# Kernel optimization log

Hardware: AMD Instinct MI355X
Metric: run time of the kernel (lower is better)

## Reference

```python
import jax, jax.numpy as jnp
import numpy as np

V, D, H, DFF, L = 32000, 256, 4, 1024, 4
B, T = 2, 2048
DK = D // H
EPS = 1e-5


def setup_inputs() -> dict:
    key = jax.random.key(0)
    ks = jax.random.split(key, 8)
    s = 0.02
    return {
        "tokens": jax.random.randint(ks[0], (B, T), 0, V),
        "embed": jax.random.normal(ks[1], (V, D), jnp.float32) * s,
        "qkv_w": jax.random.normal(ks[2], (L, 3 * D, D), jnp.float32) * s,
        "qkv_b": jnp.zeros((L, 3 * D), jnp.float32),
        "fc_w": jax.random.normal(ks[3], (L, D, D), jnp.float32) * s,
        "fc_b": jnp.zeros((L, D), jnp.float32),
        "ln1_s": jnp.ones((L, D), jnp.float32),
        "ln1_b": jnp.zeros((L, D), jnp.float32),
        "w1": jax.random.normal(ks[4], (L, DFF, D), jnp.float32) * s,
        "b1": jnp.zeros((L, DFF), jnp.float32),
        "w2": jax.random.normal(ks[5], (L, D, DFF), jnp.float32) * s,
        "b2": jnp.zeros((L, D), jnp.float32),
        "ln2_s": jnp.ones((L, D), jnp.float32),
        "ln2_b": jnp.zeros((L, D), jnp.float32),
        "lnf_s": jnp.ones((D,), jnp.float32),
        "lnf_b": jnp.zeros((D,), jnp.float32),
        "out_w": jax.random.normal(ks[6], (V, D), jnp.float32) * s,
        "out_b": jnp.zeros((V,), jnp.float32),
    }


def _layernorm(x, s, b):
    mu = jnp.mean(x, axis=-1, keepdims=True)
    var = jnp.mean(jnp.square(x - mu), axis=-1, keepdims=True)
    return (x - mu) * jax.lax.rsqrt(var + EPS) * s + b


def _pos_encoding(t, d):
    pos = jnp.arange(t, dtype=jnp.float32)[:, None]
    div = jnp.exp(jnp.arange(0, d, 2, dtype=jnp.float32) * (-np.log(10000.0) / d))
    pe = jnp.zeros((t, d), jnp.float32)
    pe = pe.at[:, 0::2].set(jnp.sin(pos * div))
    pe = pe.at[:, 1::2].set(jnp.cos(pos * div))
    return pe


def reference(tokens, embed, qkv_w, qkv_b, fc_w, fc_b, ln1_s, ln1_b,
              w1, b1, w2, b2, ln2_s, ln2_b, lnf_s, lnf_b, out_w, out_b):
    b, t = tokens.shape
    x = embed[tokens] + _pos_encoding(t, D)[None]  # [B,T,D]
    causal = jnp.tril(jnp.ones((t, t), bool))
    scale = 1.0 / np.sqrt(DK)
    for l in range(L):
        # --- attention ---
        qkv = jnp.einsum('btd,ed->bte', x, qkv_w[l]) + qkv_b[l]  # [B,T,3D]
        qkv = qkv.reshape(b, t, 3, H, DK)
        q, k, v = qkv[:, :, 0], qkv[:, :, 1], qkv[:, :, 2]  # [B,T,H,DK]
        scores = jnp.einsum('bqhd,bkhd->bhqk', q, k) * scale
        scores = jnp.where(causal, scores, -jnp.inf)
        attn = jax.nn.softmax(scores, axis=-1)
        o = jnp.einsum('bhqk,bkhd->bqhd', attn, v).reshape(b, t, D)
        o = jnp.einsum('btd,ed->bte', o, fc_w[l]) + fc_b[l]
        x = _layernorm(x + o, ln1_s[l], ln1_b[l])
        # --- feed-forward ---
        h = jax.nn.relu(jnp.einsum('btd,fd->btf', x, w1[l]) + b1[l])
        f = jnp.einsum('btf,df->btd', h, w2[l]) + b2[l]
        x = _layernorm(x + f, ln2_s[l], ln2_b[l])
    x = _layernorm(x, lnf_s, lnf_b)
    logits = jnp.einsum('btd,vd->btv', x, out_w) + out_b
    return logits
```

## Files before the change

### kernel.cpp

```cpp
#include <hip/hip_runtime.h>
#include <math.h>

typedef __attribute__((ext_vector_type(8))) short bf16x8;
typedef __attribute__((ext_vector_type(4))) float f32x4;
typedef __attribute__((ext_vector_type(4))) unsigned int u32x4;
typedef __attribute__((ext_vector_type(4))) unsigned short u16x4;

static constexpr int Tn = 2048;
static constexpr int Dm = 256;
static constexpr int NHn = 4;
static constexpr int Ln = 4;
static constexpr int DFFn = 1024;
static constexpr int Vn = 32000;
static constexpr int BTn = 4096;

__device__ __forceinline__ unsigned short f2bf(float f) {
  unsigned int u = __float_as_uint(f);
  u += 0x7fffu + ((u >> 16) & 1u);
  return (unsigned short)(u >> 16);
}

__device__ __forceinline__ void gld_lds16(const unsigned short* g, unsigned short* l) {
  __builtin_amdgcn_global_load_lds((const __attribute__((address_space(1))) unsigned int*)g,
                                   (__attribute__((address_space(3))) unsigned int*)l, 16, 0, 0);
}

__global__ __launch_bounds__(256) void cvt_f2bf(const float* __restrict__ in,
                                                unsigned short* __restrict__ out, int n) {
  int i = (blockIdx.x * 256 + threadIdx.x) * 4;
  if (i >= n) return;
  float4 v = *reinterpret_cast<const float4*>(in + i);
  u16x4 o;
  o[0] = f2bf(v.x); o[1] = f2bf(v.y); o[2] = f2bf(v.z); o[3] = f2bf(v.w);
  *reinterpret_cast<u16x4*>(out + i) = o;
}

__global__ __launch_bounds__(256) void embed_pos(const int* __restrict__ tokens,
                                                 const float* __restrict__ emb,
                                                 float* __restrict__ xf,
                                                 unsigned short* __restrict__ xb) {
  int idx = blockIdx.x * 256 + threadIdx.x;
  int bt = idx >> 8, d = idx & 255;
  int t = bt & (Tn - 1);
  int tok = tokens[bt];
  float v = emb[(size_t)tok * Dm + d];
  int i2 = d & ~1;
  float dv = expf((float)i2 * (-0.03597789207803249f));
  float arg = (float)t * dv;
  float pe = (d & 1) ? cosf(arg) : sinf(arg);
  float x = v + pe;
  xf[idx] = x;
  xb[idx] = f2bf(x);
}

__global__ __launch_bounds__(256) void add_ln(const float* __restrict__ addend,
                                              const float* __restrict__ gam,
                                              const float* __restrict__ bet,
                                              float* __restrict__ xf,
                                              unsigned short* __restrict__ xb) {
  int row = blockIdx.x, d = threadIdx.x;
  __shared__ float red[8];
  size_t off = (size_t)row * Dm + d;
  float u = xf[off];
  if (addend) u += addend[off];
  float tsum = u;
  #pragma unroll
  for (int o = 32; o > 0; o >>= 1) tsum += __shfl_xor(tsum, o);
  int w = d >> 6, lane = d & 63;
  if (lane == 0) red[w] = tsum;
  __syncthreads();
  float mean = (red[0] + red[1] + red[2] + red[3]) * (1.f / 256.f);
  float df = u - mean;
  float vsum = df * df;
  #pragma unroll
  for (int o = 32; o > 0; o >>= 1) vsum += __shfl_xor(vsum, o);
  if (lane == 0) red[4 + w] = vsum;
  __syncthreads();
  float var = (red[4] + red[5] + red[6] + red[7]) * (1.f / 256.f);
  float y = df * rsqrtf(var + 1e-5f) * gam[d] + bet[d];
  xf[off] = y;
  xb[off] = f2bf(y);
}

__global__ __launch_bounds__(256) void attn_mfma(const unsigned short* __restrict__ qkv,
                                                 unsigned short* __restrict__ ob) {
  int lin = blockIdx.y * gridDim.x + blockIdx.x;
  int wg = (lin & 7) * 32 + (lin >> 3);
  int qb = wg & 31, bh = wg >> 5;
  int b = bh >> 2, h = bh & 3;
  int q0 = qb * 64;
  int tid = threadIdx.x;
  int lane = tid & 63, w = tid >> 6;
  int l15 = lane & 15, quad = lane >> 4;

  __shared__ __align__(16) unsigned short Ps[4][16 * 64];
  __shared__ __align__(16) unsigned short Vt[64 * 64];

  const size_t rowQ = (size_t)(b * Tn + q0 + w * 16 + l15) * 768 + h * 64 + quad * 8;
  bf16x8 aq0 = *reinterpret_cast<const bf16x8*>(qkv + rowQ);
  bf16x8 aq1 = *reinterpret_cast<const bf16x8*>(qkv + rowQ + 32);

  float m_i[4], l_i[4];
  f32x4 oacc[4];
  #pragma unroll
  for (int i = 0; i < 4; i++) { m_i[i] = -INFINITY; l_i[i] = 0.f; oacc[i] = (f32x4){0.f, 0.f, 0.f, 0.f}; }

  for (int jt = 0; jt <= qb; jt++) {
    int j0 = jt * 64;
    __syncthreads();
    {
      int kv = tid & 63, g = tid >> 6;
      const unsigned short* vsrc = qkv + (size_t)(b * Tn + j0 + kv) * 768 + 512 + h * 64 + g * 16;
      bf16x8 v0 = *reinterpret_cast<const bf16x8*>(vsrc);
      bf16x8 v1 = *reinterpret_cast<const bf16x8*>(vsrc + 8);
      char* vb = (char*)Vt;
      #pragma unroll
      for (int j = 0; j < 8; j++) {
        int dk = g * 16 + j;
        *(unsigned short*)(vb + (((dk * 128 + kv * 2)) ^ ((dk & 7) << 4))) = (unsigned short)v0[j];
      }
      #pragma unroll
      for (int j = 0; j < 8; j++) {
        int dk = g * 16 + 8 + j;
        *(unsigned short*)(vb + (((dk * 128 + kv * 2)) ^ ((dk & 7) << 4))) = (unsigned short)v1[j];
      }
    }
    __syncthreads();

    f32x4 sc[4];
    const size_t rowK = (size_t)(b * Tn + j0 + l15) * 768 + 256 + h * 64 + quad * 8;
    #pragma unroll
    for (int f = 0; f < 4; f++) {
      bf16x8 bk0 = *reinterpret_cast<const bf16x8*>(qkv + rowK + (size_t)f * 16 * 768);
      bf16x8 bk1 = *reinterpret_cast<const bf16x8*>(qkv + rowK + (size_t)f * 16 * 768 + 32);
      f32x4 a = (f32x4){0.f, 0.f, 0.f, 0.f};
      a = __builtin_amdgcn_mfma_f32_16x16x32_bf16(aq0, bk0, a, 0, 0, 0);
      a = __builtin_amdgcn_mfma_f32_16x16x32_bf16(aq1, bk1, a, 0, 0, 0);
      sc[f] = a;
    }

    bool diag = (jt == qb);
    float alpha[4];
    #pragma unroll
    for (int rr = 0; rr < 4; rr++) {
      int qg = q0 + w * 16 + quad * 4 + rr;
      float sv[4];
      #pragma unroll
      for (int f = 0; f < 4; f++) {
        sv[f] = sc[f][rr] * 0.125f;
        if (diag && (j0 + f * 16 + l15 > qg)) sv[f] = -INFINITY;
      }
      float mx = fmaxf(fmaxf(sv[0], sv[1]), fmaxf(sv[2], sv[3]));
      #pragma unroll
      for (int o = 8; o > 0; o >>= 1) mx = fmaxf(mx, __shfl_xor(mx, o));
      float mnew = fmaxf(m_i[rr], mx);
      float p[4], ps = 0.f;
      #pragma unroll
      for (int f = 0; f < 4; f++) { p[f] = __expf(sv[f] - mnew); ps += p[f]; }
      #pragma unroll
      for (int o = 8; o > 0; o >>= 1) ps += __shfl_xor(ps, o);
      alpha[rr] = __expf(m_i[rr] - mnew);
      l_i[rr] = l_i[rr] * alpha[rr] + ps;
      m_i[rr] = mnew;
      int qq = quad * 4 + rr;
      char* pb = (char*)Ps[w];
      #pragma unroll
      for (int f = 0; f < 4; f++)
        *(unsigned short*)(pb + (((qq * 128 + (f * 16 + l15) * 2)) ^ ((qq & 7) << 4))) = f2bf(p[f]);
    }

    #pragma unroll
    for (int ni = 0; ni < 4; ni++)
      #pragma unroll
      for (int rr = 0; rr < 4; rr++) oacc[ni][rr] *= alpha[rr];

    bf16x8 pa[2];
    {
      char* pb = (char*)Ps[w];
      #pragma unroll
      for (int kc = 0; kc < 2; kc++)
        pa[kc] = *reinterpret_cast<const bf16x8*>(
            pb + (((l15 * 128 + kc * 64 + quad * 16)) ^ ((l15 & 7) << 4)));
    }
    char* vb = (char*)Vt;
    #pragma unroll
    for (int ni = 0; ni < 4; ni++) {
      int dk = ni * 16 + l15;
      #pragma unroll
      for (int kc = 0; kc < 2; kc++) {
        bf16x8 bv = *reinterpret_cast<const bf16x8*>(
            vb + (((dk * 128 + kc * 64 + quad * 16)) ^ ((dk & 7) << 4)));
        oacc[ni] = __builtin_amdgcn_mfma_f32_16x16x32_bf16(pa[kc], bv, oacc[ni], 0, 0, 0);
      }
    }
  }

  #pragma unroll
  for (int ni = 0; ni < 4; ni++) {
    #pragma unroll
    for (int rr = 0; rr < 4; rr++) {
      int qg = q0 + w * 16 + quad * 4 + rr;
      float o = oacc[ni][rr] / l_i[rr];
      ob[(size_t)(b * Tn + qg) * Dm + h * 64 + ni * 16 + l15] = f2bf(o);
    }
  }
}

template <int BM, int EPI>
__global__ __launch_bounds__(256) void gemm_bt(const unsigned short* __restrict__ A,
                                               const unsigned short* __restrict__ W,
                                               const float* __restrict__ bias,
                                               float* __restrict__ Cf,
                                               unsigned short* __restrict__ Cb,
                                               int M, int N, int K) {
  constexpr int MI = BM / 32;
  __shared__ __align__(16) unsigned short As[BM * 32];
  __shared__ __align__(16) unsigned short Bs[128 * 32];
  int tid = threadIdx.x;
  int lane = tid & 63, w = tid >> 6;
  int wm = (w >> 1) * (BM / 2), wn = (w & 1) * 64;
  int r = lane & 15, quad = lane >> 4;

  int nwg = gridDim.x * gridDim.y;
  int lin = blockIdx.y * gridDim.x + blockIdx.x;
  int xcd = lin & 7, pos = lin >> 3;
  int qch = nwg >> 3, rch = nwg & 7;
  int wg = (xcd < rch ? xcd * (qch + 1) : rch * (qch + 1) + (xcd - rch) * qch) + pos;
  int m0 = (wg % gridDim.x) * BM;
  int n0 = (wg / gridDim.x) * 128;

  f32x4 acc[MI][4];
  #pragma unroll
  for (int i = 0; i < MI; i++)
    #pragma unroll
    for (int j = 0; j < 4; j++) acc[i][j] = (f32x4){0.f, 0.f, 0.f, 0.f};

  int lrow = lane >> 2;
  int lcol = (lane & 3) * 8;
  for (int k0 = 0; k0 < K; k0 += 32) {
    __syncthreads();
    #pragma unroll
    for (int i = 0; i < BM / 64; i++) {
      int rowA = i * 64 + w * 16;
      gld_lds16(A + (size_t)(m0 + rowA + lrow) * K + k0 + lcol, &As[rowA * 32]);
    }
    #pragma unroll
    for (int i = 0; i < 2; i++) {
      int rowB = i * 64 + w * 16;
      gld_lds16(W + (size_t)(n0 + rowB + lrow) * K + k0 + lcol, &Bs[rowB * 32]);
    }
    __syncthreads();
    bf16x8 af[MI], bfr[4];
    #pragma unroll
    for (int mi = 0; mi < MI; mi++)
      af[mi] = *reinterpret_cast<const bf16x8*>(&As[(wm + mi * 16 + r) * 32 + quad * 8]);
    #pragma unroll
    for (int ni = 0; ni < 4; ni++)
      bfr[ni] = *reinterpret_cast<const bf16x8*>(&Bs[(wn + ni * 16 + r) * 32 + quad * 8]);
    #pragma unroll
    for (int mi = 0; mi < MI; mi++)
      #pragma unroll
      for (int ni = 0; ni < 4; ni++)
        acc[mi][ni] = __builtin_amdgcn_mfma_f32_16x16x32_bf16(af[mi], bfr[ni], acc[mi][ni], 0, 0, 0);
  }
  #pragma unroll
  for (int mi = 0; mi < MI; mi++) {
    #pragma unroll
    for (int ni = 0; ni < 4; ni++) {
      int n = n0 + wn + ni * 16 + r;
      float bv = bias[n];
      #pragma unroll
      for (int rr = 0; rr < 4; rr++) {
        int m = m0 + wm + mi * 16 + quad * 4 + rr;
        float v = acc[mi][ni][rr] + bv;
        if (EPI == 0) {
          Cf[(size_t)m * N + n] = v;
        } else if (EPI == 1) {
          Cb[(size_t)m * N + n] = f2bf(fmaxf(v, 0.f));
        } else {
          Cb[(size_t)m * N + n] = f2bf(v);
        }
      }
    }
  }
}

extern "C" void kernel_launch(void* const* d_in, const int* in_sizes, int n_in,
                              void* d_out, int out_size, void* d_ws, size_t ws_size,
                              hipStream_t stream) {
  (void)in_sizes; (void)n_in; (void)out_size; (void)ws_size;
  const int* tokens = (const int*)d_in[0];
  const float* emb = (const float*)d_in[1];
  const float* qkv_w = (const float*)d_in[2];
  const float* qkv_b = (const float*)d_in[3];
  const float* fc_w = (const float*)d_in[4];
  const float* fc_b = (const float*)d_in[5];
  const float* ln1_s = (const float*)d_in[6];
  const float* ln1_b = (const float*)d_in[7];
  const float* w1 = (const float*)d_in[8];
  const float* b1 = (const float*)d_in[9];
  const float* w2 = (const float*)d_in[10];
  const float* b2 = (const float*)d_in[11];
  const float* ln2_s = (const float*)d_in[12];
  const float* ln2_b = (const float*)d_in[13];
  const float* lnf_s = (const float*)d_in[14];
  const float* lnf_b = (const float*)d_in[15];
  const float* out_w = (const float*)d_in[16];
  const float* out_b = (const float*)d_in[17];
  float* logits = (float*)d_out;

  char* p = (char*)d_ws;
  auto carve = [&](size_t bytes) {
    char* r = p;
    p += (bytes + 255) & ~(size_t)255;
    return r;
  };
  float* xf = (float*)carve((size_t)BTn * Dm * 4);
  unsigned short* xb = (unsigned short*)carve((size_t)BTn * Dm * 2);
  unsigned short* qkvb = (unsigned short*)carve((size_t)BTn * 768 * 2);
  unsigned short* obb = (unsigned short*)carve((size_t)BTn * Dm * 2);
  float* of = (float*)carve((size_t)BTn * Dm * 4);
  unsigned short* hb = (unsigned short*)carve((size_t)BTn * DFFn * 2);
  float* ff = (float*)carve((size_t)BTn * Dm * 4);
  unsigned short* wqkvb = (unsigned short*)carve((size_t)Ln * 768 * Dm * 2);
  unsigned short* wfcb = (unsigned short*)carve((size_t)Ln * Dm * Dm * 2);
  unsigned short* w1b = (unsigned short*)carve((size_t)Ln * DFFn * Dm * 2);
  unsigned short* w2b = (unsigned short*)carve((size_t)Ln * Dm * DFFn * 2);
  unsigned short* outwb = (unsigned short*)carve((size_t)Vn * Dm * 2);

  auto cvt = [&](const float* src, unsigned short* dst, int n) {
    cvt_f2bf<<<dim3((n / 4 + 255) / 256), dim3(256), 0, stream>>>(src, dst, n);
  };
  cvt(qkv_w, wqkvb, Ln * 768 * Dm);
  cvt(fc_w, wfcb, Ln * Dm * Dm);
  cvt(w1, w1b, Ln * DFFn * Dm);
  cvt(w2, w2b, Ln * Dm * DFFn);
  cvt(out_w, outwb, Vn * Dm);

  embed_pos<<<dim3(BTn), dim3(256), 0, stream>>>(tokens, emb, xf, xb);

  for (int l = 0; l < Ln; l++) {
    gemm_bt<64, 2><<<dim3(BTn / 64, 768 / 128), dim3(256), 0, stream>>>(
        xb, wqkvb + (size_t)l * 768 * Dm, qkv_b + l * 768, nullptr, qkvb, BTn, 768, Dm);
    attn_mfma<<<dim3(Tn / 64, 2 * NHn), dim3(256), 0, stream>>>(qkvb, obb);
    gemm_bt<64, 0><<<dim3(BTn / 64, Dm / 128), dim3(256), 0, stream>>>(
        obb, wfcb + (size_t)l * Dm * Dm, fc_b + l * Dm, of, nullptr, BTn, Dm, Dm);
    add_ln<<<dim3(BTn), dim3(256), 0, stream>>>(of, ln1_s + l * Dm, ln1_b + l * Dm, xf, xb);
    gemm_bt<128, 1><<<dim3(BTn / 128, DFFn / 128), dim3(256), 0, stream>>>(
        xb, w1b + (size_t)l * DFFn * Dm, b1 + l * DFFn, nullptr, hb, BTn, DFFn, Dm);
    gemm_bt<64, 0><<<dim3(BTn / 64, Dm / 128), dim3(256), 0, stream>>>(
        hb, w2b + (size_t)l * Dm * DFFn, b2 + l * Dm, ff, nullptr, BTn, Dm, DFFn);
    add_ln<<<dim3(BTn), dim3(256), 0, stream>>>(ff, ln2_s + l * Dm, ln2_b + l * Dm, xf, xb);
  }
  add_ln<<<dim3(BTn), dim3(256), 0, stream>>>(nullptr, lnf_s, lnf_b, xf, xb);

  gemm_bt<128, 0><<<dim3(BTn / 128, Vn / 128), dim3(256), 0, stream>>>(
      xb, outwb, out_b, logits, nullptr, BTn, Vn, Dm);
}
```

Before: 1.253 ms.

## Load GEMM operands directly to registers and fuse weight conversions into one launch

Replaces the LDS-staged GEMM with one where each wave loads its MFMA fragments straight from global memory into registers. K becomes a compile-time parameter with an unrolled k-loop, and all __syncthreads barriers are removed. The five weight-conversion launches are merged into one kernel, and the fc/w2 GEMMs use smaller M tiles to get more blocks. The aim is to cut barrier and launch overhead. The risk is redundant global and L2 traffic, because waves sharing rows no longer share loaded tiles, and the 16-byte fragment loads are strided.

```diff
diff --git a/kernel.cpp b/kernel.cpp
--- a/kernel.cpp
+++ b/kernel.cpp
@@ -20,19 +20,25 @@
   return (unsigned short)(u >> 16);
 }
 
-__device__ __forceinline__ void gld_lds16(const unsigned short* g, unsigned short* l) {
-  __builtin_amdgcn_global_load_lds((const __attribute__((address_space(1))) unsigned int*)g,
-                                   (__attribute__((address_space(3))) unsigned int*)l, 16, 0, 0);
-}
-
-__global__ __launch_bounds__(256) void cvt_f2bf(const float* __restrict__ in,
-                                                unsigned short* __restrict__ out, int n) {
-  int i = (blockIdx.x * 256 + threadIdx.x) * 4;
-  if (i >= n) return;
-  float4 v = *reinterpret_cast<const float4*>(in + i);
+__global__ __launch_bounds__(256) void cvt_all(const float* __restrict__ s0, unsigned short* __restrict__ d0,
+                                               const float* __restrict__ s1, unsigned short* __restrict__ d1,
+                                               const float* __restrict__ s2, unsigned short* __restrict__ d2,
+                                               const float* __restrict__ s3, unsigned short* __restrict__ d3,
+                                               const float* __restrict__ s4, unsigned short* __restrict__ d4,
+                                               int e0, int e1, int e2, int e3, int e4) {
+  int g = blockIdx.x * 256 + threadIdx.x;
+  if (g >= e4) return;
+  const float* s; unsigned short* d; int base;
+  if (g < e0)      { s = s0; d = d0; base = 0; }
+  else if (g < e1) { s = s1; d = d1; base = e0; }
+  else if (g < e2) { s = s2; d = d2; base = e1; }
+  else if (g < e3) { s = s3; d = d3; base = e2; }
+  else             { s = s4; d = d4; base = e3; }
+  int i = (g - base) * 4;
+  float4 v = *reinterpret_cast<const float4*>(s + i);
   u16x4 o;
   o[0] = f2bf(v.x); o[1] = f2bf(v.y); o[2] = f2bf(v.z); o[3] = f2bf(v.w);
-  *reinterpret_cast<u16x4*>(out + i) = o;
+  *reinterpret_cast<u16x4*>(d + i) = o;
 }
 
 __global__ __launch_bounds__(256) void embed_pos(const int* __restrict__ tokens,
@@ -206,28 +212,30 @@
   }
 }
 
-template <int BM, int EPI>
-__global__ __launch_bounds__(256) void gemm_bt(const unsigned short* __restrict__ A,
+template <int BM, int K, int EPI>
+__global__ __launch_bounds__(256) void gemm_rf(const unsigned short* __restrict__ A,
                                                const unsigned short* __restrict__ W,
                                                const float* __restrict__ bias,
                                                float* __restrict__ Cf,
                                                unsigned short* __restrict__ Cb,
-                                               int M, int N, int K) {
+                                               int N) {
   constexpr int MI = BM / 32;
-  __shared__ __align__(16) unsigned short As[BM * 32];
-  __shared__ __align__(16) unsigned short Bs[128 * 32];
   int tid = threadIdx.x;
   int lane = tid & 63, w = tid >> 6;
   int wm = (w >> 1) * (BM / 2), wn = (w & 1) * 64;
   int r = lane & 15, quad = lane >> 4;
 
-  int nwg = gridDim.x * gridDim.y;
-  int lin = blockIdx.y * gridDim.x + blockIdx.x;
+  int gx = gridDim.x;
+  int nwg = gx * gridDim.y;
+  int lin = blockIdx.y * gx + blockIdx.x;
   int xcd = lin & 7, pos = lin >> 3;
   int qch = nwg >> 3, rch = nwg & 7;
   int wg = (xcd < rch ? xcd * (qch + 1) : rch * (qch + 1) + (xcd - rch) * qch) + pos;
-  int m0 = (wg % gridDim.x) * BM;
-  int n0 = (wg / gridDim.x) * 128;
+  int m0 = (wg % gx) * BM;
+  int n0 = (wg / gx) * 128;
+
+  const unsigned short* Ap = A + (size_t)(m0 + wm + r) * K + quad * 8;
+  const unsigned short* Wp = W + (size_t)(n0 + wn + r) * K + quad * 8;
 
   f32x4 acc[MI][4];
   #pragma unroll
@@ -235,34 +243,22 @@
     #pragma unroll
     for (int j = 0; j < 4; j++) acc[i][j] = (f32x4){0.f, 0.f, 0.f, 0.f};
 
-  int lrow = lane >> 2;
-  int lcol = (lane & 3) * 8;
+  #pragma unroll 8
   for (int k0 = 0; k0 < K; k0 += 32) {
-    __syncthreads();
-    #pragma unroll
-    for (int i = 0; i < BM / 64; i++) {
-      int rowA = i * 64 + w * 16;
-      gld_lds16(A + (size_t)(m0 + rowA + lrow) * K + k0 + lcol, &As[rowA * 32]);
-    }
-    #pragma unroll
-    for (int i = 0; i < 2; i++) {
-      int rowB = i * 64 + w * 16;
-      gld_lds16(W + (size_t)(n0 + rowB + lrow) * K + k0 + lcol, &Bs[rowB * 32]);
-    }
-    __syncthreads();
     bf16x8 af[MI], bfr[4];
     #pragma unroll
     for (int mi = 0; mi < MI; mi++)
-      af[mi] = *reinterpret_cast<const bf16x8*>(&As[(wm + mi * 16 + r) * 32 + quad * 8]);
+      af[mi] = *reinterpret_cast<const bf16x8*>(Ap + (size_t)mi * 16 * K + k0);
     #pragma unroll
     for (int ni = 0; ni < 4; ni++)
-      bfr[ni] = *reinterpret_cast<const bf16x8*>(&Bs[(wn + ni * 16 + r) * 32 + quad * 8]);
+      bfr[ni] = *reinterpret_cast<const bf16x8*>(Wp + (size_t)ni * 16 * K + k0);
     #pragma unroll
     for (int mi = 0; mi < MI; mi++)
       #pragma unroll
       for (int ni = 0; ni < 4; ni++)
         acc[mi][ni] = __builtin_amdgcn_mfma_f32_16x16x32_bf16(af[mi], bfr[ni], acc[mi][ni], 0, 0, 0);
   }
+
   #pragma unroll
   for (int mi = 0; mi < MI; mi++) {
     #pragma unroll
@@ -328,32 +324,33 @@
   unsigned short* w2b = (unsigned short*)carve((size_t)Ln * Dm * DFFn * 2);
   unsigned short* outwb = (unsigned short*)carve((size_t)Vn * Dm * 2);
 
-  auto cvt = [&](const float* src, unsigned short* dst, int n) {
-    cvt_f2bf<<<dim3((n / 4 + 255) / 256), dim3(256), 0, stream>>>(src, dst, n);
-  };
-  cvt(qkv_w, wqkvb, Ln * 768 * Dm);
-  cvt(fc_w, wfcb, Ln * Dm * Dm);
-  cvt(w1, w1b, Ln * DFFn * Dm);
-  cvt(w2, w2b, Ln * Dm * DFFn);
-  cvt(out_w, outwb, Vn * Dm);
+  {
+    int c0 = Ln * 768 * Dm / 4;
+    int c1 = c0 + Ln * Dm * Dm / 4;
+    int c2 = c1 + Ln * DFFn * Dm / 4;
+    int c3 = c2 + Ln * Dm * DFFn / 4;
+    int c4 = c3 + Vn * Dm / 4;
+    cvt_all<<<dim3((c4 + 255) / 256), dim3(256), 0, stream>>>(
+        qkv_w, wqkvb, fc_w, wfcb, w1, w1b, w2, w2b, out_w, outwb, c0, c1, c2, c3, c4);
+  }
 
   embed_pos<<<dim3(BTn), dim3(256), 0, stream>>>(tokens, emb, xf, xb);
 
   for (int l = 0; l < Ln; l++) {
-    gemm_bt<64, 2><<<dim3(BTn / 64, 768 / 128), dim3(256), 0, stream>>>(
-        xb, wqkvb + (size_t)l * 768 * Dm, qkv_b + l * 768, nullptr, qkvb, BTn, 768, Dm);
+    gemm_rf<64, 256, 2><<<dim3(BTn / 64, 768 / 128), dim3(256), 0, stream>>>(
+        xb, wqkvb + (size_t)l * 768 * Dm, qkv_b + l * 768, nullptr, qkvb, 768);
     attn_mfma<<<dim3(Tn / 64, 2 * NHn), dim3(256), 0, stream>>>(qkvb, obb);
-    gemm_bt<64, 0><<<dim3(BTn / 64, Dm / 128), dim3(256), 0, stream>>>(
-        obb, wfcb + (size_t)l * Dm * Dm, fc_b + l * Dm, of, nullptr, BTn, Dm, Dm);
+    gemm_rf<32, 256, 0><<<dim3(BTn / 32, Dm / 128), dim3(256), 0, stream>>>(
+        obb, wfcb + (size_t)l * Dm * Dm, fc_b + l * Dm, of, nullptr, Dm);
     add_ln<<<dim3(BTn), dim3(256), 0, stream>>>(of, ln1_s + l * Dm, ln1_b + l * Dm, xf, xb);
-    gemm_bt<128, 1><<<dim3(BTn / 128, DFFn / 128), dim3(256), 0, stream>>>(
-        xb, w1b + (size_t)l * DFFn * Dm, b1 + l * DFFn, nullptr, hb, BTn, DFFn, Dm);
-    gemm_bt<64, 0><<<dim3(BTn / 64, Dm / 128), dim3(256), 0, stream>>>(
-        hb, w2b + (size_t)l * Dm * DFFn, b2 + l * Dm, ff, nullptr, BTn, Dm, DFFn);
+    gemm_rf<64, 256, 1><<<dim3(BTn / 64, DFFn / 128), dim3(256), 0, stream>>>(
+        xb, w1b + (size_t)l * DFFn * Dm, b1 + l * DFFn, nullptr, hb, DFFn);
+    gemm_rf<32, 1024, 0><<<dim3(BTn / 32, Dm / 128), dim3(256), 0, stream>>>(
+        hb, w2b + (size_t)l * Dm * DFFn, b2 + l * Dm, ff, nullptr, Dm);
     add_ln<<<dim3(BTn), dim3(256), 0, stream>>>(ff, ln2_s + l * Dm, ln2_b + l * Dm, xf, xb);
   }
   add_ln<<<dim3(BTn), dim3(256), 0, stream>>>(nullptr, lnf_s, lnf_b, xf, xb);
 
-  gemm_bt<128, 0><<<dim3(BTn / 128, Vn / 128), dim3(256), 0, stream>>>(
-      xb, outwb, out_b, logits, nullptr, BTn, Vn, Dm);
-}
+  gemm_rf<128, 256, 0><<<dim3(BTn / 128, Vn / 128), dim3(256), 0, stream>>>(
+      xb, outwb, out_b, logits, nullptr, Vn);
+}
```

Result: slower. 1.393 ms (+11.1%).
